# Kernel tuning notes

Measured on AMD Instinct MI355X. Metric: run time of the kernel, lower is better.

## Reference

```python
import jax, jax.numpy as jnp
import numpy as np

N = 50000      # nodes
E = 500000     # edges (includes N self-loops)
DIN = 512
DOUT = 256
NEG_SLOPE = 0.01  # torch nn.LeakyReLU default


def setup_inputs() -> dict:
    key = jax.random.key(0)
    k1, k2, k3, k4, k5 = jax.random.split(key, 5)
    x = jax.random.normal(k1, (N, DIN), dtype=jnp.float32)
    # xavier_normal_ with gain=1.414
    std_W = 1.414 * np.sqrt(2.0 / (DIN + DOUT))
    W = jax.random.normal(k2, (DIN, DOUT), dtype=jnp.float32) * std_W
    std_a = 1.414 * np.sqrt(2.0 / (1 + 2 * DOUT))
    a = jax.random.normal(k3, (2 * DOUT,), dtype=jnp.float32) * std_a
    # first N edges are self-loops so every row-sum is nonzero
    loops = jnp.arange(N, dtype=jnp.int32)
    edge_src = jnp.concatenate([loops, jax.random.randint(k4, (E - N,), 0, N, dtype=jnp.int32)])
    edge_dst = jnp.concatenate([loops, jax.random.randint(k5, (E - N,), 0, N, dtype=jnp.int32)])
    return {"x": x, "W": W, "a": a, "edge_src": edge_src, "edge_dst": edge_dst}


def reference(x, W, a, edge_src, edge_dst):
    n = x.shape[0]
    d = W.shape[1]
    h = x @ W  # [N, DOUT]
    # a . [h_src ; h_dst] decomposed per-node, then gathered per-edge
    s_src = h @ a[:d]   # [N]
    s_dst = h @ a[d:]   # [N]
    score = s_src[edge_src] + s_dst[edge_dst]          # [E]
    e = jnp.exp(-jax.nn.leaky_relu(score, NEG_SLOPE))  # [E]
    # sparse softmax denominator: spmm(edge, e, ones) == segment sum over src
    e_rowsum = jax.ops.segment_sum(e, edge_src, num_segments=n)            # [N]
    # numerator: spmm(edge, e, h) == sum_j e_ij * h_j per row i
    h_prime = jax.ops.segment_sum(e[:, None] * h[edge_dst], edge_src, num_segments=n)  # [N, DOUT]
    h_prime = h_prime / e_rowsum[:, None]
    return jax.nn.elu(h_prime)  # concat=True branch
```

## Files before the change

### kernel.cpp

```cpp
#include <hip/hip_runtime.h>
#include <math.h>

#define DIN 512
#define DOUT 256
#define NEG_SLOPE 0.01f
#define GBM 256
#define GBN 64

typedef __attribute__((ext_vector_type(8))) short bf16x8;
typedef __attribute__((ext_vector_type(4))) float f32x4;
typedef __attribute__((ext_vector_type(4))) unsigned int u32x4;

__device__ __forceinline__ unsigned short f2bf(float f) {
    unsigned int u = __float_as_uint(f);
    unsigned int r = (u + 0x7FFFu + ((u >> 16) & 1u)) >> 16;
    return (unsigned short)r;
}
__device__ __forceinline__ float bf2f(unsigned short u) {
    return __uint_as_float(((unsigned int)u) << 16);
}
__device__ __forceinline__ unsigned int cvtpk(float lo, float hi) {
    unsigned int r;
    asm("v_cvt_pk_bf16_f32 %0, %1, %2" : "=v"(r) : "v"(lo), "v"(hi));
    return r;
}
__device__ __forceinline__ void gload16(const void* g, void* l) {
    __builtin_amdgcn_global_load_lds(
        (const __attribute__((address_space(1))) void*)g,
        (__attribute__((address_space(3))) void*)l, 16, 0, 0);
}

__global__ void prep(const float* __restrict__ W, unsigned short* __restrict__ Wt,
                     int* __restrict__ deg, float* __restrict__ s_src,
                     float* __restrict__ s_dst, int N) {
    int t = blockIdx.x * blockDim.x + threadIdx.x;
    if (t < DIN * DOUT) {
        int k = t & (DIN - 1);
        int c = t >> 9;
        Wt[t] = f2bf(W[(size_t)k * DOUT + c]);
    }
    if (t < N) { deg[t] = 0; s_src[t] = 0.f; s_dst[t] = 0.f; }
}

__global__ __launch_bounds__(512) void gemm_k(const float* __restrict__ x,
                                              const unsigned short* __restrict__ Wt,
                                              unsigned short* __restrict__ hb,
                                              const float* __restrict__ av,
                                              float* __restrict__ s_src,
                                              float* __restrict__ s_dst, int M) {
    __shared__ unsigned char Bs[65536];
    const int t = threadIdx.x;
    const int lane = t & 63;
    const int wv = t >> 6;
    const int m0 = blockIdx.x * GBM;
    const int n0 = blockIdx.y * GBN;

#pragma unroll
    for (int it = 0; it < 8; ++it) {
        int c = wv * 8 + it;
        const unsigned short* src = Wt + (size_t)(n0 + c) * DIN + ((lane ^ (c & 7)) * 8);
        gload16(src, Bs + c * 1024);
    }

    float as_[4], ad_[4];
#pragma unroll
    for (int cf = 0; cf < 4; ++cf) {
        int col = n0 + cf * 16 + (lane & 15);
        as_[cf] = av[col];
        ad_[cf] = av[DOUT + col];
    }

    f32x4 acc[2][4] = {};
    const int g = lane >> 4;
    int row0 = m0 + wv * 32 + (lane & 15);
    int r0 = min(row0, M - 1);
    int r1 = min(row0 + 16, M - 1);
    const float* pA0 = x + (size_t)r0 * DIN + g * 8;
    const float* pA1 = x + (size_t)r1 * DIN + g * 8;

    __syncthreads();

#pragma unroll 4
    for (int ks = 0; ks < DIN / 32; ++ks) {
        bf16x8 afr[2];
        {
            f32x4 v0 = *(const f32x4*)(pA0 + ks * 32);
            f32x4 v1 = *(const f32x4*)(pA0 + ks * 32 + 4);
            u32x4 p;
            p.x = cvtpk(v0.x, v0.y); p.y = cvtpk(v0.z, v0.w);
            p.z = cvtpk(v1.x, v1.y); p.w = cvtpk(v1.z, v1.w);
            afr[0] = *(bf16x8*)&p;
            f32x4 w0 = *(const f32x4*)(pA1 + ks * 32);
            f32x4 w1 = *(const f32x4*)(pA1 + ks * 32 + 4);
            u32x4 q;
            q.x = cvtpk(w0.x, w0.y); q.y = cvtpk(w0.z, w0.w);
            q.z = cvtpk(w1.x, w1.y); q.w = cvtpk(w1.z, w1.w);
            afr[1] = *(bf16x8*)&q;
        }
#pragma unroll
        for (int cf = 0; cf < 4; ++cf) {
            int col = cf * 16 + (lane & 15);
            bf16x8 bfr = *(const bf16x8*)(Bs + col * 1024 + (((ks * 4 + g) ^ (col & 7)) << 4));
            acc[0][cf] = __builtin_amdgcn_mfma_f32_16x16x32_bf16(afr[0], bfr, acc[0][cf], 0, 0, 0);
            acc[1][cf] = __builtin_amdgcn_mfma_f32_16x16x32_bf16(afr[1], bfr, acc[1][cf], 0, 0, 0);
        }
    }

#pragma unroll
    for (int rf = 0; rf < 2; ++rf) {
#pragma unroll
        for (int j = 0; j < 4; ++j) {
            int row = m0 + wv * 32 + rf * 16 + g * 4 + j;
            float ps = 0.f, pd = 0.f;
#pragma unroll
            for (int cf = 0; cf < 4; ++cf) {
                float v = acc[rf][cf][j];
                ps += v * as_[cf];
                pd += v * ad_[cf];
            }
#pragma unroll
            for (int off = 1; off < 16; off <<= 1) {
                ps += __shfl_xor(ps, off);
                pd += __shfl_xor(pd, off);
            }
            if (row < M) {
#pragma unroll
                for (int cf = 0; cf < 4; ++cf)
                    hb[(size_t)row * DOUT + n0 + cf * 16 + (lane & 15)] = f2bf(acc[rf][cf][j]);
                if ((lane & 15) == 0) {
                    atomicAdd(&s_src[row], ps);
                    atomicAdd(&s_dst[row], pd);
                }
            }
        }
    }
}

__global__ void hist_k(const int* __restrict__ src, int* __restrict__ deg, int E) {
    int i = blockIdx.x * blockDim.x + threadIdx.x;
    if (i < E) atomicAdd(&deg[src[i]], 1);
}

__global__ __launch_bounds__(256) void block_sum(const int* __restrict__ deg, int* __restrict__ bsum, int N) {
    __shared__ int wsum[4];
    int b = blockIdx.x, t = threadIdx.x;
    int idx = b * 1024 + t * 4;
    int s = 0;
    if (idx + 3 < N) {
        int4 v = *(const int4*)(deg + idx);
        s = v.x + v.y + v.z + v.w;
    } else {
        for (int i = 0; i < 4; i++) if (idx + i < N) s += deg[idx + i];
    }
#pragma unroll
    for (int off = 32; off > 0; off >>= 1) s += __shfl_xor(s, off);
    if ((t & 63) == 0) wsum[t >> 6] = s;
    __syncthreads();
    if (t == 0) bsum[b] = wsum[0] + wsum[1] + wsum[2] + wsum[3];
}

__global__ void scan_tops(const int* __restrict__ bsum, int* __restrict__ boff,
                          int* __restrict__ rowptr, int nb, int N, int E) {
    int t = threadIdx.x;
    int v = (t < nb) ? bsum[t] : 0;
    int x = v;
#pragma unroll
    for (int off = 1; off < 64; off <<= 1) {
        int y = __shfl_up(x, off);
        if (t >= off) x += y;
    }
    if (t < nb) boff[t] = x - v;
    if (t == 0) rowptr[N] = E;
}

__global__ __launch_bounds__(256) void scan_blk(const int* __restrict__ deg, const int* __restrict__ boff,
                                                int* __restrict__ rowptr, int* __restrict__ cursor, int N) {
    __shared__ int wsum[4];
    int b = blockIdx.x, t = threadIdx.x;
    int idx = b * 1024 + t * 4;
    int v0 = 0, v1 = 0, v2 = 0, v3 = 0;
    if (idx + 3 < N) {
        int4 v = *(const int4*)(deg + idx);
        v0 = v.x; v1 = v.y; v2 = v.z; v3 = v.w;
    } else if (idx < N) {
        v0 = deg[idx];
        if (idx + 1 < N) v1 = deg[idx + 1];
        if (idx + 2 < N) v2 = deg[idx + 2];
    }
    int s = v0 + v1 + v2 + v3;
    int lane = t & 63, wid = t >> 6;
    int x = s;
#pragma unroll
    for (int off = 1; off < 64; off <<= 1) {
        int y = __shfl_up(x, off);
        if (lane >= off) x += y;
    }
    if (lane == 63) wsum[wid] = x;
    __syncthreads();
    int add = boff[b];
    for (int ww = 0; ww < wid; ++ww) add += wsum[ww];
    int e0 = add + x - s;
    int e1 = e0 + v0, e2 = e1 + v1, e3 = e2 + v2;
    if (idx < N)     { rowptr[idx] = e0;     cursor[idx] = e0; }
    if (idx + 1 < N) { rowptr[idx + 1] = e1; cursor[idx + 1] = e1; }
    if (idx + 2 < N) { rowptr[idx + 2] = e2; cursor[idx + 2] = e2; }
    if (idx + 3 < N) { rowptr[idx + 3] = e3; cursor[idx + 3] = e3; }
}

__global__ void edge_k(const int* __restrict__ src, const int* __restrict__ dst,
                       const float* __restrict__ s_src, const float* __restrict__ s_dst,
                       int* __restrict__ cursor, int2* __restrict__ csr, int E) {
    int i = blockIdx.x * blockDim.x + threadIdx.x;
    if (i >= E) return;
    int s = src[i], d = dst[i];
    float sc = s_src[s] + s_dst[d];
    float lrv = sc > 0.f ? sc : NEG_SLOPE * sc;
    float ev = __expf(-lrv);
    int pos = atomicAdd(&cursor[s], 1);
    csr[pos] = make_int2(d, __float_as_int(ev));
}

__global__ __launch_bounds__(256) void gather_k(const unsigned short* __restrict__ hb,
                                                const int* __restrict__ rowptr,
                                                const int2* __restrict__ csr,
                                                float* __restrict__ out, int N) {
    int gt = blockIdx.x * blockDim.x + threadIdx.x;
    int w = gt >> 6;
    int lane = threadIdx.x & 63;
    if (w >= N) return;
    int s0 = rowptr[w], s1 = rowptr[w + 1];
    float a0 = 0.f, a1 = 0.f, a2 = 0.f, a3 = 0.f, rs = 0.f;
    for (int base = s0; base < s1; base += 64) {
        int cnt = min(64, s1 - base);
        int dv = 0; float ev = 0.f;
        if (lane < cnt) {
            int2 p = csr[base + lane];
            dv = p.x; ev = __int_as_float(p.y);
        }
        int jj = 0;
        for (; jj + 4 <= cnt; jj += 4) {
            int d0 = __shfl(dv, jj), d1 = __shfl(dv, jj + 1), d2 = __shfl(dv, jj + 2), d3 = __shfl(dv, jj + 3);
            float e0 = __shfl(ev, jj), e1 = __shfl(ev, jj + 1), e2 = __shfl(ev, jj + 2), e3 = __shfl(ev, jj + 3);
            ushort4 h0 = *(const ushort4*)(hb + (size_t)d0 * DOUT + lane * 4);
            ushort4 h1 = *(const ushort4*)(hb + (size_t)d1 * DOUT + lane * 4);
            ushort4 h2 = *(const ushort4*)(hb + (size_t)d2 * DOUT + lane * 4);
            ushort4 h3 = *(const ushort4*)(hb + (size_t)d3 * DOUT + lane * 4);
            a0 += e0 * bf2f(h0.x) + e1 * bf2f(h1.x) + e2 * bf2f(h2.x) + e3 * bf2f(h3.x);
            a1 += e0 * bf2f(h0.y) + e1 * bf2f(h1.y) + e2 * bf2f(h2.y) + e3 * bf2f(h3.y);
            a2 += e0 * bf2f(h0.z) + e1 * bf2f(h1.z) + e2 * bf2f(h2.z) + e3 * bf2f(h3.z);
            a3 += e0 * bf2f(h0.w) + e1 * bf2f(h1.w) + e2 * bf2f(h2.w) + e3 * bf2f(h3.w);
            rs += e0 + e1 + e2 + e3;
        }
        for (; jj < cnt; ++jj) {
            int d0 = __shfl(dv, jj);
            float e0 = __shfl(ev, jj);
            ushort4 h0 = *(const ushort4*)(hb + (size_t)d0 * DOUT + lane * 4);
            a0 += e0 * bf2f(h0.x);
            a1 += e0 * bf2f(h0.y);
            a2 += e0 * bf2f(h0.z);
            a3 += e0 * bf2f(h0.w);
            rs += e0;
        }
    }
    float inv = 1.f / rs;
    float4 v;
    v.x = a0 * inv; v.y = a1 * inv; v.z = a2 * inv; v.w = a3 * inv;
    v.x = v.x > 0.f ? v.x : __expf(v.x) - 1.f;
    v.y = v.y > 0.f ? v.y : __expf(v.y) - 1.f;
    v.z = v.z > 0.f ? v.z : __expf(v.z) - 1.f;
    v.w = v.w > 0.f ? v.w : __expf(v.w) - 1.f;
    *(float4*)(out + (size_t)w * DOUT + lane * 4) = v;
}

extern "C" void kernel_launch(void* const* d_in, const int* in_sizes, int n_in,
                              void* d_out, int out_size, void* d_ws, size_t ws_size,
                              hipStream_t stream) {
    const float* x = (const float*)d_in[0];
    const float* W = (const float*)d_in[1];
    const float* a = (const float*)d_in[2];
    const int* edge_src = (const int*)d_in[3];
    const int* edge_dst = (const int*)d_in[4];

    const int N = in_sizes[0] / DIN;
    const int E = in_sizes[3];
    const int nb = (N + 1023) / 1024;

    char* ws = (char*)d_ws;
    size_t off = 0;
    auto alloc = [&](size_t bytes) {
        void* p = ws + off;
        off += (bytes + 15) & ~(size_t)15;
        return p;
    };
    unsigned short* hb = (unsigned short*)alloc((size_t)N * DOUT * 2);
    unsigned short* Wt = (unsigned short*)alloc((size_t)DIN * DOUT * 2);
    int* rowptr = (int*)alloc((size_t)(N + 1) * 4);
    int* deg = (int*)alloc((size_t)N * 4);
    int* cursor = (int*)alloc((size_t)N * 4);
    float* s_src = (float*)alloc((size_t)N * 4);
    float* s_dst = (float*)alloc((size_t)N * 4);
    int2* csr = (int2*)alloc((size_t)E * 8);
    int* bsum = (int*)alloc((size_t)nb * 4);
    int* boff = (int*)alloc((size_t)nb * 4);
    (void)ws_size;

    float* out = (float*)d_out;

    prep<<<(DIN * DOUT + 255) / 256, 256, 0, stream>>>(W, Wt, deg, s_src, s_dst, N);
    hist_k<<<(E + 255) / 256, 256, 0, stream>>>(edge_src, deg, E);
    dim3 ggrid((N + GBM - 1) / GBM, DOUT / GBN);
    gemm_k<<<ggrid, 512, 0, stream>>>(x, Wt, hb, a, s_src, s_dst, N);
    block_sum<<<nb, 256, 0, stream>>>(deg, bsum, N);
    scan_tops<<<1, 64, 0, stream>>>(bsum, boff, rowptr, nb, N, E);
    scan_blk<<<nb, 256, 0, stream>>>(deg, boff, rowptr, cursor, N);
    edge_k<<<(E + 255) / 256, 256, 0, stream>>>(edge_src, edge_dst, s_src, s_dst,
                                                cursor, csr, E);
    gather_k<<<(N + 3) / 4, 256, 0, stream>>>(hb, rowptr, csr, out, N);
}
```

Baseline: 179.0 us.

## Retile GEMM to full-width 128-row blocks with K-chunked W staging

The projection GEMM now computes a 128x256 output tile per block instead of 256x64, streaming W through shared memory in four K-chunks. This reduces how many times each fp32 x row is loaded from global memory and converted to bf16. The trade-off is extra barriers per chunk with no double buffering, plus a launch-bounds occupancy hint.

Result: faster. 156.2 us (-12.7%).

```diff
diff --git a/kernel.cpp b/kernel.cpp
--- a/kernel.cpp
+++ b/kernel.cpp
@@ -4,8 +4,6 @@
 #define DIN 512
 #define DOUT 256
 #define NEG_SLOPE 0.01f
-#define GBM 256
-#define GBN 64
 
 typedef __attribute__((ext_vector_type(8))) short bf16x8;
 typedef __attribute__((ext_vector_type(4))) float f32x4;
@@ -42,78 +40,82 @@
     if (t < N) { deg[t] = 0; s_src[t] = 0.f; s_dst[t] = 0.f; }
 }
 
-__global__ __launch_bounds__(512) void gemm_k(const float* __restrict__ x,
-                                              const unsigned short* __restrict__ Wt,
-                                              unsigned short* __restrict__ hb,
-                                              const float* __restrict__ av,
-                                              float* __restrict__ s_src,
-                                              float* __restrict__ s_dst, int M) {
+__global__ __launch_bounds__(512, 4) void gemm_k(const float* __restrict__ x,
+                                                 const unsigned short* __restrict__ Wt,
+                                                 unsigned short* __restrict__ hb,
+                                                 const float* __restrict__ av,
+                                                 float* __restrict__ s_src,
+                                                 float* __restrict__ s_dst, int M) {
     __shared__ unsigned char Bs[65536];
     const int t = threadIdx.x;
     const int lane = t & 63;
+    const int l15 = lane & 15;
+    const int g = lane >> 4;
     const int wv = t >> 6;
-    const int m0 = blockIdx.x * GBM;
-    const int n0 = blockIdx.y * GBN;
-
-#pragma unroll
-    for (int it = 0; it < 8; ++it) {
-        int c = wv * 8 + it;
-        const unsigned short* src = Wt + (size_t)(n0 + c) * DIN + ((lane ^ (c & 7)) * 8);
-        gload16(src, Bs + c * 1024);
-    }
-
-    float as_[4], ad_[4];
-#pragma unroll
-    for (int cf = 0; cf < 4; ++cf) {
-        int col = n0 + cf * 16 + (lane & 15);
-        as_[cf] = av[col];
-        ad_[cf] = av[DOUT + col];
-    }
-
-    f32x4 acc[2][4] = {};
-    const int g = lane >> 4;
-    int row0 = m0 + wv * 32 + (lane & 15);
+    const int wr = wv >> 1;
+    const int wc = wv & 1;
+    const int m0 = blockIdx.x * 128;
+
+    f32x4 acc[2][8] = {};
+    int row0 = m0 + wr * 32 + l15;
     int r0 = min(row0, M - 1);
     int r1 = min(row0 + 16, M - 1);
     const float* pA0 = x + (size_t)r0 * DIN + g * 8;
     const float* pA1 = x + (size_t)r1 * DIN + g * 8;
 
-    __syncthreads();
-
-#pragma unroll 4
-    for (int ks = 0; ks < DIN / 32; ++ks) {
-        bf16x8 afr[2];
-        {
-            f32x4 v0 = *(const f32x4*)(pA0 + ks * 32);
-            f32x4 v1 = *(const f32x4*)(pA0 + ks * 32 + 4);
-            u32x4 p;
-            p.x = cvtpk(v0.x, v0.y); p.y = cvtpk(v0.z, v0.w);
-            p.z = cvtpk(v1.x, v1.y); p.w = cvtpk(v1.z, v1.w);
-            afr[0] = *(bf16x8*)&p;
-            f32x4 w0 = *(const f32x4*)(pA1 + ks * 32);
-            f32x4 w1 = *(const f32x4*)(pA1 + ks * 32 + 4);
-            u32x4 q;
-            q.x = cvtpk(w0.x, w0.y); q.y = cvtpk(w0.z, w0.w);
-            q.z = cvtpk(w1.x, w1.y); q.w = cvtpk(w1.z, w1.w);
-            afr[1] = *(bf16x8*)&q;
-        }
-#pragma unroll
-        for (int cf = 0; cf < 4; ++cf) {
-            int col = cf * 16 + (lane & 15);
-            bf16x8 bfr = *(const bf16x8*)(Bs + col * 1024 + (((ks * 4 + g) ^ (col & 7)) << 4));
-            acc[0][cf] = __builtin_amdgcn_mfma_f32_16x16x32_bf16(afr[0], bfr, acc[0][cf], 0, 0, 0);
-            acc[1][cf] = __builtin_amdgcn_mfma_f32_16x16x32_bf16(afr[1], bfr, acc[1][cf], 0, 0, 0);
-        }
-    }
-
+    for (int kc = 0; kc < 4; ++kc) {
+        if (kc) __syncthreads();
+#pragma unroll
+        for (int it = 0; it < 8; ++it) {
+            int fs = it * 512 + t;
+            int col = fs >> 4;
+            int slot = (fs & 15) ^ (col & 15);
+            gload16(Wt + (size_t)col * DIN + kc * 128 + slot * 8, Bs + fs * 16);
+        }
+        __syncthreads();
+#pragma unroll
+        for (int ksl = 0; ksl < 4; ++ksl) {
+            int ks = kc * 4 + ksl;
+            bf16x8 afr0, afr1;
+            {
+                f32x4 v0 = *(const f32x4*)(pA0 + ks * 32);
+                f32x4 v1 = *(const f32x4*)(pA0 + ks * 32 + 4);
+                u32x4 p;
+                p.x = cvtpk(v0.x, v0.y); p.y = cvtpk(v0.z, v0.w);
+                p.z = cvtpk(v1.x, v1.y); p.w = cvtpk(v1.z, v1.w);
+                afr0 = *(bf16x8*)&p;
+                f32x4 w0 = *(const f32x4*)(pA1 + ks * 32);
+                f32x4 w1 = *(const f32x4*)(pA1 + ks * 32 + 4);
+                u32x4 q;
+                q.x = cvtpk(w0.x, w0.y); q.y = cvtpk(w0.z, w0.w);
+                q.z = cvtpk(w1.x, w1.y); q.w = cvtpk(w1.z, w1.w);
+                afr1 = *(bf16x8*)&q;
+            }
+#pragma unroll
+            for (int cf = 0; cf < 8; ++cf) {
+                int col = wc * 128 + cf * 16 + l15;
+                bf16x8 bfr = *(const bf16x8*)(Bs + col * 256 + (((ksl * 4 + g) ^ (col & 15)) << 4));
+                acc[0][cf] = __builtin_amdgcn_mfma_f32_16x16x32_bf16(afr0, bfr, acc[0][cf], 0, 0, 0);
+                acc[1][cf] = __builtin_amdgcn_mfma_f32_16x16x32_bf16(afr1, bfr, acc[1][cf], 0, 0, 0);
+            }
+        }
+    }
+
+    float as_[8], ad_[8];
+#pragma unroll
+    for (int cf = 0; cf < 8; ++cf) {
+        int col = wc * 128 + cf * 16 + l15;
+        as_[cf] = av[col];
+        ad_[cf] = av[DOUT + col];
+    }
 #pragma unroll
     for (int rf = 0; rf < 2; ++rf) {
 #pragma unroll
         for (int j = 0; j < 4; ++j) {
-            int row = m0 + wv * 32 + rf * 16 + g * 4 + j;
+            int row = m0 + wr * 32 + rf * 16 + g * 4 + j;
             float ps = 0.f, pd = 0.f;
 #pragma unroll
-            for (int cf = 0; cf < 4; ++cf) {
+            for (int cf = 0; cf < 8; ++cf) {
                 float v = acc[rf][cf][j];
                 ps += v * as_[cf];
                 pd += v * ad_[cf];
@@ -125,9 +127,9 @@
             }
             if (row < M) {
 #pragma unroll
-                for (int cf = 0; cf < 4; ++cf)
-                    hb[(size_t)row * DOUT + n0 + cf * 16 + (lane & 15)] = f2bf(acc[rf][cf][j]);
-                if ((lane & 15) == 0) {
+                for (int cf = 0; cf < 8; ++cf)
+                    hb[(size_t)row * DOUT + wc * 128 + cf * 16 + l15] = f2bf(acc[rf][cf][j]);
+                if (l15 == 0) {
                     atomicAdd(&s_src[row], ps);
                     atomicAdd(&s_dst[row], pd);
                 }
@@ -308,8 +310,7 @@
 
     prep<<<(DIN * DOUT + 255) / 256, 256, 0, stream>>>(W, Wt, deg, s_src, s_dst, N);
     hist_k<<<(E + 255) / 256, 256, 0, stream>>>(edge_src, deg, E);
-    dim3 ggrid((N + GBM - 1) / GBM, DOUT / GBN);
-    gemm_k<<<ggrid, 512, 0, stream>>>(x, Wt, hb, a, s_src, s_dst, N);
+    gemm_k<<<(N + 127) / 128, 512, 0, stream>>>(x, Wt, hb, a, s_src, s_dst, N);
     block_sum<<<nb, 256, 0, stream>>>(deg, bsum, N);
     scan_tops<<<1, 64, 0, stream>>>(bsum, boff, rowptr, nb, N, E);
     scan_blk<<<nb, 256, 0, stream>>>(deg, boff, rowptr, cursor, N);
```

## Retile GEMM so each block covers all output columns, reading x once

Applied to the files above, without the earlier changes.

Changes the projection GEMM from 256x64 tiles with W staged in LDS to 32-row blocks where each of four waves covers a 64-column slice of the full 256 outputs. This removes the four-fold re-reading of the large fp32 input x across column blocks. In exchange, W fragments are read directly from global memory (relying on L2/L1 caching) with no LDS reuse, and the block shape and launch bounds change occupancy.

New measurement: 207.0 us. +15.6%, slower.

```diff
diff --git a/kernel.cpp b/kernel.cpp
--- a/kernel.cpp
+++ b/kernel.cpp
@@ -4,8 +4,6 @@
 #define DIN 512
 #define DOUT 256
 #define NEG_SLOPE 0.01f
-#define GBM 256
-#define GBN 64
 
 typedef __attribute__((ext_vector_type(8))) short bf16x8;
 typedef __attribute__((ext_vector_type(4))) float f32x4;
@@ -23,11 +21,6 @@
     unsigned int r;
     asm("v_cvt_pk_bf16_f32 %0, %1, %2" : "=v"(r) : "v"(lo), "v"(hi));
     return r;
-}
-__device__ __forceinline__ void gload16(const void* g, void* l) {
-    __builtin_amdgcn_global_load_lds(
-        (const __attribute__((address_space(1))) void*)g,
-        (__attribute__((address_space(3))) void*)l, 16, 0, 0);
 }
 
 __global__ void prep(const float* __restrict__ W, unsigned short* __restrict__ Wt,
@@ -42,75 +35,60 @@
     if (t < N) { deg[t] = 0; s_src[t] = 0.f; s_dst[t] = 0.f; }
 }
 
-__global__ __launch_bounds__(512) void gemm_k(const float* __restrict__ x,
-                                              const unsigned short* __restrict__ Wt,
-                                              unsigned short* __restrict__ hb,
-                                              const float* __restrict__ av,
-                                              float* __restrict__ s_src,
-                                              float* __restrict__ s_dst, int M) {
-    __shared__ unsigned char Bs[65536];
+__global__ __launch_bounds__(256, 4) void gemm_k(const float* __restrict__ x,
+                                                 const unsigned short* __restrict__ Wt,
+                                                 unsigned short* __restrict__ hb,
+                                                 const float* __restrict__ av,
+                                                 float* __restrict__ s_src,
+                                                 float* __restrict__ s_dst, int M) {
     const int t = threadIdx.x;
     const int lane = t & 63;
+    const int l15 = lane & 15;
+    const int g = lane >> 4;
     const int wv = t >> 6;
-    const int m0 = blockIdx.x * GBM;
-    const int n0 = blockIdx.y * GBN;
-
-#pragma unroll
-    for (int it = 0; it < 8; ++it) {
-        int c = wv * 8 + it;
-        const unsigned short* src = Wt + (size_t)(n0 + c) * DIN + ((lane ^ (c & 7)) * 8);
-        gload16(src, Bs + c * 1024);
+    const int m0 = blockIdx.x * 32;
+
+    f32x4 acc[2][4] = {};
+    int r0 = min(m0 + l15, M - 1);
+    int r1 = min(m0 + 16 + l15, M - 1);
+    const float* pA0 = x + (size_t)r0 * DIN + g * 8;
+    const float* pA1 = x + (size_t)r1 * DIN + g * 8;
+    const unsigned short* pB = Wt + (size_t)(wv * 64 + l15) * DIN + g * 8;
+
+#pragma unroll 4
+    for (int ks = 0; ks < DIN / 32; ++ks) {
+        f32x4 v0 = *(const f32x4*)(pA0 + ks * 32);
+        f32x4 v1 = *(const f32x4*)(pA0 + ks * 32 + 4);
+        f32x4 w0 = *(const f32x4*)(pA1 + ks * 32);
+        f32x4 w1 = *(const f32x4*)(pA1 + ks * 32 + 4);
+        u32x4 p;
+        p.x = cvtpk(v0.x, v0.y); p.y = cvtpk(v0.z, v0.w);
+        p.z = cvtpk(v1.x, v1.y); p.w = cvtpk(v1.z, v1.w);
+        bf16x8 afr0 = *(bf16x8*)&p;
+        u32x4 q;
+        q.x = cvtpk(w0.x, w0.y); q.y = cvtpk(w0.z, w0.w);
+        q.z = cvtpk(w1.x, w1.y); q.w = cvtpk(w1.z, w1.w);
+        bf16x8 afr1 = *(bf16x8*)&q;
+#pragma unroll
+        for (int cf = 0; cf < 4; ++cf) {
+            bf16x8 bfr = *(const bf16x8*)(pB + (size_t)cf * 16 * DIN + ks * 32);
+            acc[0][cf] = __builtin_amdgcn_mfma_f32_16x16x32_bf16(afr0, bfr, acc[0][cf], 0, 0, 0);
+            acc[1][cf] = __builtin_amdgcn_mfma_f32_16x16x32_bf16(afr1, bfr, acc[1][cf], 0, 0, 0);
+        }
     }
 
     float as_[4], ad_[4];
 #pragma unroll
     for (int cf = 0; cf < 4; ++cf) {
-        int col = n0 + cf * 16 + (lane & 15);
+        int col = wv * 64 + cf * 16 + l15;
         as_[cf] = av[col];
         ad_[cf] = av[DOUT + col];
     }
-
-    f32x4 acc[2][4] = {};
-    const int g = lane >> 4;
-    int row0 = m0 + wv * 32 + (lane & 15);
-    int r0 = min(row0, M - 1);
-    int r1 = min(row0 + 16, M - 1);
-    const float* pA0 = x + (size_t)r0 * DIN + g * 8;
-    const float* pA1 = x + (size_t)r1 * DIN + g * 8;
-
-    __syncthreads();
-
-#pragma unroll 4
-    for (int ks = 0; ks < DIN / 32; ++ks) {
-        bf16x8 afr[2];
-        {
-            f32x4 v0 = *(const f32x4*)(pA0 + ks * 32);
-            f32x4 v1 = *(const f32x4*)(pA0 + ks * 32 + 4);
-            u32x4 p;
-            p.x = cvtpk(v0.x, v0.y); p.y = cvtpk(v0.z, v0.w);
-            p.z = cvtpk(v1.x, v1.y); p.w = cvtpk(v1.z, v1.w);
-            afr[0] = *(bf16x8*)&p;
-            f32x4 w0 = *(const f32x4*)(pA1 + ks * 32);
-            f32x4 w1 = *(const f32x4*)(pA1 + ks * 32 + 4);
-            u32x4 q;
-            q.x = cvtpk(w0.x, w0.y); q.y = cvtpk(w0.z, w0.w);
-            q.z = cvtpk(w1.x, w1.y); q.w = cvtpk(w1.z, w1.w);
-            afr[1] = *(bf16x8*)&q;
-        }
-#pragma unroll
-        for (int cf = 0; cf < 4; ++cf) {
-            int col = cf * 16 + (lane & 15);
-            bf16x8 bfr = *(const bf16x8*)(Bs + col * 1024 + (((ks * 4 + g) ^ (col & 7)) << 4));
-            acc[0][cf] = __builtin_amdgcn_mfma_f32_16x16x32_bf16(afr[0], bfr, acc[0][cf], 0, 0, 0);
-            acc[1][cf] = __builtin_amdgcn_mfma_f32_16x16x32_bf16(afr[1], bfr, acc[1][cf], 0, 0, 0);
-        }
-    }
-
 #pragma unroll
     for (int rf = 0; rf < 2; ++rf) {
 #pragma unroll
         for (int j = 0; j < 4; ++j) {
-            int row = m0 + wv * 32 + rf * 16 + g * 4 + j;
+            int row = m0 + rf * 16 + g * 4 + j;
             float ps = 0.f, pd = 0.f;
 #pragma unroll
             for (int cf = 0; cf < 4; ++cf) {
@@ -126,8 +104,8 @@
             if (row < M) {
 #pragma unroll
                 for (int cf = 0; cf < 4; ++cf)
-                    hb[(size_t)row * DOUT + n0 + cf * 16 + (lane & 15)] = f2bf(acc[rf][cf][j]);
-                if ((lane & 15) == 0) {
+                    hb[(size_t)row * DOUT + wv * 64 + cf * 16 + l15] = f2bf(acc[rf][cf][j]);
+                if (l15 == 0) {
                     atomicAdd(&s_src[row], ps);
                     atomicAdd(&s_dst[row], pd);
                 }
@@ -308,8 +286,7 @@
 
     prep<<<(DIN * DOUT + 255) / 256, 256, 0, stream>>>(W, Wt, deg, s_src, s_dst, N);
     hist_k<<<(E + 255) / 256, 256, 0, stream>>>(edge_src, deg, E);
-    dim3 ggrid((N + GBM - 1) / GBM, DOUT / GBN);
-    gemm_k<<<ggrid, 512, 0, stream>>>(x, Wt, hb, a, s_src, s_dst, N);
+    gemm_k<<<(N + 31) / 32, 256, 0, stream>>>(x, Wt, hb, a, s_src, s_dst, N);
     block_sum<<<nb, 256, 0, stream>>>(deg, bsum, N);
     scan_tops<<<1, 64, 0, stream>>>(bsum, boff, rowptr, nb, N, E);
     scan_blk<<<nb, 256, 0, stream>>>(deg, boff, rowptr, cursor, N);
```
